# Kernel tuning notes

Hardware: AMD Instinct MI355X
Metric: run time of the kernel (lower is better)

The kernel has to match this reference:

```python
import jax, jax.numpy as jnp
import numpy as np

B, L, D = 8, 1024, 1024
H = 16
HD = D // H  # 64
R = 8


def setup_inputs() -> dict:
    key = jax.random.key(0)
    ks = jax.random.split(key, 12)
    s = 1.0 / np.sqrt(D)
    return {
        "x": jax.random.normal(ks[0], (B, L, D), dtype=jnp.float32),
        "Wq": jax.random.normal(ks[1], (D, D), dtype=jnp.float32) * s,
        "bq": jnp.zeros((D,), dtype=jnp.float32),
        "Wk": jax.random.normal(ks[2], (D, D), dtype=jnp.float32) * s,
        "bk": jnp.zeros((D,), dtype=jnp.float32),
        "Wv": jax.random.normal(ks[3], (D, D), dtype=jnp.float32) * s,
        "bv": jnp.zeros((D,), dtype=jnp.float32),
        "Wo": jax.random.normal(ks[4], (D, D), dtype=jnp.float32) * s,
        "bo": jnp.zeros((D,), dtype=jnp.float32),
        "Wrel": jax.random.normal(ks[5], (H, R), dtype=jnp.float32) * (1.0 / np.sqrt(H)),
        "brel": jnp.zeros((R,), dtype=jnp.float32),
    }


def reference(x, Wq, bq, Wk, bk, Wv, bv, Wo, bo, Wrel, brel):
    # Standard MHA with need_weights=True: full [B,H,L,L] attention matrix.
    def heads(t):  # [B,L,D] -> [B,H,L,HD]
        return t.reshape(B, L, H, HD).transpose(0, 2, 1, 3)

    q = heads(x @ Wq + bq)
    k = heads(x @ Wk + bk)
    v = heads(x @ Wv + bv)

    scores = jnp.einsum('bhld,bhmd->bhlm', q, k) / jnp.sqrt(jnp.float32(HD))
    attn = jax.nn.softmax(scores, axis=-1)  # [B,H,L,L]

    ctx = jnp.einsum('bhlm,bhmd->bhld', attn, v)
    ctx = ctx.transpose(0, 2, 1, 3).reshape(B, L, D)
    output = ctx @ Wo + bo  # [B,L,D]

    # head_patterns: mean of attention weights over (L, L) -> [B, H]
    head_patterns = attn.mean(axis=(2, 3))
    relation_scores = head_patterns @ Wrel + brel  # [B,R]
    return output, relation_scores
```

## Files before the change

### kernel.cpp

```cpp
#include <hip/hip_runtime.h>
#include <math.h>

using f32x4  = __attribute__((ext_vector_type(4))) float;
using bf16x8 = __attribute__((ext_vector_type(8))) short;
using us8    = __attribute__((ext_vector_type(8))) unsigned short;
using us4    = __attribute__((ext_vector_type(4))) unsigned short;

static __device__ __forceinline__ unsigned short f32_bf16(float f) {
    unsigned int u = __float_as_uint(f);
    u += 0x7fffu + ((u >> 16) & 1u);
    return (unsigned short)(u >> 16);
}

static __device__ __forceinline__ float fast_exp2(float x) {
    return __builtin_amdgcn_exp2f(x);
}

static __device__ __forceinline__ unsigned int bf16pk(float lo, float hi) {
    unsigned int r;
    asm("v_cvt_pk_bf16_f32 %0, %1, %2" : "=v"(r) : "v"(lo), "v"(hi));
    return r;
}

#define GLOADLDS16(src, dst)                                                          \
    __builtin_amdgcn_global_load_lds(                                                 \
        (const __attribute__((address_space(1))) void*)(src),                         \
        (__attribute__((address_space(3))) void*)(dst), 16, 0, 0)

__global__ __launch_bounds__(256) void conv_x_kernel(const float* __restrict__ x,
                                                     unsigned short* __restrict__ xb) {
    const int i = blockIdx.x * 256 + threadIdx.x;
    const float4 v = ((const float4*)x)[i];
    us4 o;
    o.x = f32_bf16(v.x); o.y = f32_bf16(v.y); o.z = f32_bf16(v.z); o.w = f32_bf16(v.w);
    ((us4*)xb)[i] = o;
}

__global__ __launch_bounds__(256) void conv_wT_kernel(
    const float* __restrict__ Wq, const float* __restrict__ Wk,
    const float* __restrict__ Wv, const float* __restrict__ Wo,
    unsigned short* __restrict__ wqkvT, unsigned short* __restrict__ woT) {
    __shared__ float t[32][33];
    const int z = blockIdx.z;
    const float* W = (z == 0) ? Wq : (z == 1) ? Wk : (z == 2) ? Wv : Wo;
    unsigned short* dst = (z < 3) ? (wqkvT + (size_t)z * 1024 * 1024) : woT;
    const int bx = blockIdx.x * 32, by = blockIdx.y * 32;
    const int tx = threadIdx.x & 31, ty = threadIdx.x >> 5;
#pragma unroll
    for (int i = ty; i < 32; i += 8)
        t[i][tx] = W[(size_t)(by + i) * 1024 + bx + tx];
    __syncthreads();
#pragma unroll
    for (int i = ty; i < 32; i += 8)
        dst[(size_t)(bx + i) * 1024 + by + tx] = f32_bf16(t[tx][i]);
}

template<int MODE>
__global__ __launch_bounds__(256) void gemm_bt_kernel(
    const unsigned short* __restrict__ A, const unsigned short* __restrict__ Bt,
    const float* __restrict__ bias_q, const float* __restrict__ bias_k,
    const float* __restrict__ bias_v,
    unsigned short* __restrict__ qkv, float* __restrict__ cout) {
    constexpr int K = 1024;
    __shared__ unsigned short As[128 * 64];
    __shared__ unsigned short Bs[128 * 64];
    const int tid = threadIdx.x;
    const int wid = tid >> 6, lane = tid & 63;
    const int bm = blockIdx.x * 128, bn = blockIdx.y * 128;
    const int wr = wid >> 1, wc = wid & 1;
    const int l15 = lane & 15, lg = lane >> 4;
    const int srow = lane >> 3;
    const int schunk = (lane & 7) ^ srow;

    f32x4 acc[4][4] = {};

    for (int kt = 0; kt < K / 64; ++kt) {
#pragma unroll
        for (int i = 0; i < 4; ++i) {
            const int li = wid * 4 + i;
            const unsigned short* sa =
                A + (size_t)(bm + li * 8 + srow) * K + kt * 64 + schunk * 8;
            GLOADLDS16(sa, &As[li * 512]);
            const unsigned short* sb =
                Bt + (size_t)(bn + li * 8 + srow) * K + kt * 64 + schunk * 8;
            GLOADLDS16(sb, &Bs[li * 512]);
        }
        __syncthreads();
#pragma unroll
        for (int ks = 0; ks < 2; ++ks) {
            bf16x8 af[4], bfr[4];
#pragma unroll
            for (int m = 0; m < 4; ++m) {
                const int row = wr * 64 + m * 16 + l15;
                const int c = (ks * 4 + lg) ^ (row & 7);
                af[m] = *(const bf16x8*)&As[row * 64 + c * 8];
            }
#pragma unroll
            for (int n = 0; n < 4; ++n) {
                const int row = wc * 64 + n * 16 + l15;
                const int c = (ks * 4 + lg) ^ (row & 7);
                bfr[n] = *(const bf16x8*)&Bs[row * 64 + c * 8];
            }
#pragma unroll
            for (int m = 0; m < 4; ++m)
#pragma unroll
                for (int n = 0; n < 4; ++n)
                    acc[m][n] = __builtin_amdgcn_mfma_f32_16x16x32_bf16(
                        bfr[n], af[m], acc[m][n], 0, 0, 0);
        }
        __syncthreads();
    }
    if constexpr (MODE == 0) {
        const int which = bn >> 10;
        const int hnb = (bn & 1023) + wc * 64;
        const float* bias = (which == 0) ? bias_q : (which == 1) ? bias_k : bias_v;
        if (which == 2) {
#pragma unroll
            for (int m = 0; m < 4; ++m) {
                const int gm = bm + wr * 64 + m * 16 + l15;
                const int b_ = gm >> 10, li2 = gm & 1023;
#pragma unroll
                for (int n = 0; n < 4; ++n) {
                    const int hn0 = hnb + n * 16 + lg * 4;
                    const float4 bb = *(const float4*)&bias[hn0];
                    const float vv[4] = {acc[m][n][0] + bb.x, acc[m][n][1] + bb.y,
                                         acc[m][n][2] + bb.z, acc[m][n][3] + bb.w};
#pragma unroll
                    for (int r = 0; r < 4; ++r) {
                        const int hn = hn0 + r;
                        qkv[16777216 +
                            ((size_t)(b_ * 16 + (hn >> 6)) * 64 + (hn & 63)) * 1024 +
                            li2] = f32_bf16(vv[r]);
                    }
                }
            }
        } else {
            const float qs = (which == 0) ? 0.125f * 1.44269504088896f : 1.0f;
#pragma unroll
            for (int m = 0; m < 4; ++m) {
                const int gm = bm + wr * 64 + m * 16 + l15;
                const size_t rowbase =
                    (((size_t)which * 128 + (gm >> 10) * 16) * 1024 + (gm & 1023)) * 64;
#pragma unroll
                for (int n = 0; n < 4; ++n) {
                    const int hn0 = hnb + n * 16 + lg * 4;
                    const float4 bb = *(const float4*)&bias[hn0];
                    const unsigned int w01 = bf16pk((acc[m][n][0] + bb.x) * qs,
                                                    (acc[m][n][1] + bb.y) * qs);
                    const unsigned int w23 = bf16pk((acc[m][n][2] + bb.z) * qs,
                                                    (acc[m][n][3] + bb.w) * qs);
                    uint2 t; t.x = w01; t.y = w23;
                    *(uint2*)&qkv[rowbase + (size_t)(hn0 >> 6) * 65536 + (hn0 & 63)] = t;
                }
            }
        }
    } else {
#pragma unroll
        for (int m = 0; m < 4; ++m) {
            const int gm = bm + wr * 64 + m * 16 + l15;
#pragma unroll
            for (int n = 0; n < 4; ++n) {
                const int gn0 = bn + wc * 64 + n * 16 + lg * 4;
                const float4 bb = *(const float4*)&bias_q[gn0];
                float4 o;
                o.x = acc[m][n][0] + bb.x; o.y = acc[m][n][1] + bb.y;
                o.z = acc[m][n][2] + bb.z; o.w = acc[m][n][3] + bb.w;
                *(float4*)&cout[(size_t)gm * 1024 + gn0] = o;
            }
        }
    }
}

__global__ __launch_bounds__(512) void attn_kernel(
    const unsigned short* __restrict__ qkv, unsigned short* __restrict__ ctx) {
    __shared__ unsigned short Ks[2][4096];
    __shared__ unsigned short VTs[2][4096];
    __shared__ unsigned short Ps[8][1024];
    const int bh = blockIdx.x, qt = blockIdx.y;
    const int b = bh >> 4, h = bh & 15;
    const unsigned short* Qp  = qkv + (size_t)bh * 65536;
    const unsigned short* Kp  = qkv + 8388608  + (size_t)bh * 65536;
    const unsigned short* VTp = qkv + 16777216 + (size_t)bh * 65536;
    const int tid = threadIdx.x, wid = tid >> 6, lane = tid & 63;
    const int l15 = lane & 15, lg = lane >> 4;
    const int q0 = qt * 128 + wid * 16;
    const int srow = lane >> 3;
    const int schunk = (lane & 7) ^ srow;

    bf16x8 qf[2];
#pragma unroll
    for (int ks = 0; ks < 2; ++ks)
        qf[ks] = *(const bf16x8*)(Qp + (size_t)(q0 + l15) * 64 + ks * 32 + lg * 8);

    f32x4 oacc[4] = {};
    float lrow = 0.f;

    int koff[4][2], poff_r[2], poff_w[4];
#pragma unroll
    for (int nf = 0; nf < 4; ++nf)
#pragma unroll
        for (int ks = 0; ks < 2; ++ks) {
            const int row = nf * 16 + l15;
            koff[nf][ks] = row * 64 + (((ks * 4 + lg) ^ (row & 7)) * 8);
        }
#pragma unroll
    for (int ks = 0; ks < 2; ++ks)
        poff_r[ks] = l15 * 64 + (((ks * 4 + lg) ^ (l15 & 7)) * 8);
#pragma unroll
    for (int nf = 0; nf < 4; ++nf) {
        const int cchunk = nf * 2 + (lg >> 1);
        poff_w[nf] = l15 * 64 + ((cchunk ^ (l15 & 7)) * 8) + (lg & 1) * 4;
    }
    unsigned short* Pw = &Ps[wid][0];

#define ATTN_STAGE(KT, BB)                                                            \
    do {                                                                              \
        GLOADLDS16(Kp + (size_t)((KT) * 64 + wid * 8 + srow) * 64 + schunk * 8,       \
                   &Ks[BB][wid * 512]);                                               \
        GLOADLDS16(VTp + (size_t)(wid * 8 + srow) * 1024 + (KT) * 64 + schunk * 8,    \
                   &VTs[BB][wid * 512]);                                              \
    } while (0)

    ATTN_STAGE(0, 0);
    for (int kt = 0; kt < 16; ++kt) {
        const int cur = kt & 1;
        if (kt < 15) {
            ATTN_STAGE(kt + 1, cur ^ 1);
            asm volatile("s_waitcnt vmcnt(2)" ::: "memory");
        } else {
            asm volatile("s_waitcnt vmcnt(0)" ::: "memory");
        }
        __builtin_amdgcn_s_barrier();

        const unsigned short* Kb = &Ks[cur][0];
        const unsigned short* Vb = &VTs[cur][0];

        f32x4 sacc[4] = {};
        __builtin_amdgcn_s_setprio(1);
#pragma unroll
        for (int ks = 0; ks < 2; ++ks)
#pragma unroll
            for (int nf = 0; nf < 4; ++nf) {
                const bf16x8 kf = *(const bf16x8*)&Kb[koff[nf][ks]];
                sacc[nf] = __builtin_amdgcn_mfma_f32_16x16x32_bf16(
                    kf, qf[ks], sacc[nf], 0, 0, 0);
            }
        __builtin_amdgcn_s_setprio(0);

        float rsa = 0.f, rsb = 0.f;
#pragma unroll
        for (int nf = 0; nf < 4; ++nf) {
            const float p0 = fast_exp2(sacc[nf][0]);
            const float p1 = fast_exp2(sacc[nf][1]);
            const float p2 = fast_exp2(sacc[nf][2]);
            const float p3 = fast_exp2(sacc[nf][3]);
            rsa += p0 + p1; rsb += p2 + p3;
            uint2 t; t.x = bf16pk(p0, p1); t.y = bf16pk(p2, p3);
            *(uint2*)&Pw[poff_w[nf]] = t;
        }
        lrow += rsa + rsb;

        __builtin_amdgcn_s_setprio(1);
#pragma unroll
        for (int ks = 0; ks < 2; ++ks) {
            const bf16x8 pf = *(const bf16x8*)&Pw[poff_r[ks]];
#pragma unroll
            for (int nf = 0; nf < 4; ++nf) {
                const bf16x8 vf = *(const bf16x8*)&Vb[koff[nf][ks]];
                oacc[nf] = __builtin_amdgcn_mfma_f32_16x16x32_bf16(
                    vf, pf, oacc[nf], 0, 0, 0);
            }
        }
        __builtin_amdgcn_s_setprio(0);

        __builtin_amdgcn_s_barrier();
    }
#undef ATTN_STAGE

    lrow += __shfl_xor(lrow, 16);
    lrow += __shfl_xor(lrow, 32);
    const float rl = 1.0f / lrow;

#pragma unroll
    for (int nf = 0; nf < 4; ++nf) {
        uint2 t;
        t.x = bf16pk(oacc[nf][0] * rl, oacc[nf][1] * rl);
        t.y = bf16pk(oacc[nf][2] * rl, oacc[nf][3] * rl);
        *(uint2*)&ctx[((size_t)(b * 1024 + q0 + l15)) * 1024 + h * 64 + nf * 16 +
                      lg * 4] = t;
    }
}

__global__ __launch_bounds__(64) void relation_kernel(
    const float* __restrict__ Wrel, const float* __restrict__ brel,
    float* __restrict__ out) {
    const int t = threadIdx.x;
    const int r = t & 7;
    float s = 0.f;
#pragma unroll
    for (int hh = 0; hh < 16; ++hh) s += Wrel[hh * 8 + r];
    out[8 * 1024 * 1024 + t] = s * (1.0f / 1024.0f) + brel[r];
}

extern "C" void kernel_launch(void* const* d_in, const int* in_sizes, int n_in,
                              void* d_out, int out_size, void* d_ws, size_t ws_size,
                              hipStream_t stream) {
    (void)in_sizes; (void)n_in; (void)out_size; (void)ws_size;
    const float* x    = (const float*)d_in[0];
    const float* Wq   = (const float*)d_in[1];
    const float* bq   = (const float*)d_in[2];
    const float* Wk   = (const float*)d_in[3];
    const float* bk   = (const float*)d_in[4];
    const float* Wv   = (const float*)d_in[5];
    const float* bv   = (const float*)d_in[6];
    const float* Wo   = (const float*)d_in[7];
    const float* bo   = (const float*)d_in[8];
    const float* Wrel = (const float*)d_in[9];
    const float* brel = (const float*)d_in[10];
    float* out = (float*)d_out;

    char* ws = (char*)d_ws;
    unsigned short* xb    = (unsigned short*)ws;
    unsigned short* wqkvT = (unsigned short*)(ws + 16777216);
    unsigned short* woT   = (unsigned short*)(ws + 16777216 + 6291456);
    unsigned short* qkv   = (unsigned short*)(ws + 16777216 + 6291456 + 2097152);
    unsigned short* ctx   = xb;

    conv_x_kernel<<<8192, 256, 0, stream>>>(x, xb);
    conv_wT_kernel<<<dim3(32, 32, 4), 256, 0, stream>>>(Wq, Wk, Wv, Wo, wqkvT, woT);
    gemm_bt_kernel<0><<<dim3(64, 24), 256, 0, stream>>>(
        xb, wqkvT, bq, bk, bv, qkv, nullptr);
    attn_kernel<<<dim3(128, 8), 512, 0, stream>>>(qkv, ctx);
    gemm_bt_kernel<1><<<dim3(64, 8), 256, 0, stream>>>(
        ctx, woT, bo, nullptr, nullptr, nullptr, out);
    relation_kernel<<<1, 64, 0, stream>>>(Wrel, brel, out);
}
```

Before: 164.0 us.

## Load V fragments straight from global into registers, drop V LDS staging

The attention kernel no longer stages the transposed V tile through double-buffered LDS. Each wave now loads its V MFMA operands directly from global memory into registers every iteration, which halves LDS use and removes the V ds_reads. The launch bounds also request 4 blocks of 512 threads per CU. In exchange, every wave of the block fetches the same V tile, so cache traffic for V rises eightfold. The __syncthreads at the loop end likely waits on the prefetched K load, reducing overlap, and the tighter register budget could force spills.

```diff
diff --git a/kernel.cpp b/kernel.cpp
--- a/kernel.cpp
+++ b/kernel.cpp
@@ -149,8 +149,8 @@
                                                     (acc[m][n][1] + bb.y) * qs);
                     const unsigned int w23 = bf16pk((acc[m][n][2] + bb.z) * qs,
                                                     (acc[m][n][3] + bb.w) * qs);
-                    uint2 t; t.x = w01; t.y = w23;
-                    *(uint2*)&qkv[rowbase + (size_t)(hn0 >> 6) * 65536 + (hn0 & 63)] = t;
+                    uint2 t2; t2.x = w01; t2.y = w23;
+                    *(uint2*)&qkv[rowbase + (size_t)(hn0 >> 6) * 65536 + (hn0 & 63)] = t2;
                 }
             }
         }
@@ -171,10 +171,9 @@
     }
 }
 
-__global__ __launch_bounds__(512) void attn_kernel(
+__global__ __launch_bounds__(512, 4) void attn_kernel(
     const unsigned short* __restrict__ qkv, unsigned short* __restrict__ ctx) {
     __shared__ unsigned short Ks[2][4096];
-    __shared__ unsigned short VTs[2][4096];
     __shared__ unsigned short Ps[8][1024];
     const int bh = blockIdx.x, qt = blockIdx.y;
     const int b = bh >> 4, h = bh & 15;
@@ -212,29 +211,27 @@
         poff_w[nf] = l15 * 64 + ((cchunk ^ (l15 & 7)) * 8) + (lg & 1) * 4;
     }
     unsigned short* Pw = &Ps[wid][0];
+    const unsigned short* vsrc = VTp + (size_t)l15 * 1024 + lg * 8;
 
 #define ATTN_STAGE(KT, BB)                                                            \
-    do {                                                                              \
-        GLOADLDS16(Kp + (size_t)((KT) * 64 + wid * 8 + srow) * 64 + schunk * 8,       \
-                   &Ks[BB][wid * 512]);                                               \
-        GLOADLDS16(VTp + (size_t)(wid * 8 + srow) * 1024 + (KT) * 64 + schunk * 8,    \
-                   &VTs[BB][wid * 512]);                                              \
-    } while (0)
+    GLOADLDS16(Kp + (size_t)((KT) * 64 + wid * 8 + srow) * 64 + schunk * 8,           \
+               &Ks[BB][wid * 512])
 
     ATTN_STAGE(0, 0);
+    __syncthreads();
     for (int kt = 0; kt < 16; ++kt) {
         const int cur = kt & 1;
-        if (kt < 15) {
-            ATTN_STAGE(kt + 1, cur ^ 1);
-            asm volatile("s_waitcnt vmcnt(2)" ::: "memory");
-        } else {
-            asm volatile("s_waitcnt vmcnt(0)" ::: "memory");
-        }
-        __builtin_amdgcn_s_barrier();
+        if (kt < 15) ATTN_STAGE(kt + 1, cur ^ 1);
+
+        bf16x8 vf[4][2];
+#pragma unroll
+        for (int nf = 0; nf < 4; ++nf)
+#pragma unroll
+            for (int ks = 0; ks < 2; ++ks)
+                vf[nf][ks] = *(const bf16x8*)(vsrc + (size_t)nf * 16384 + kt * 64 +
+                                              ks * 32);
 
         const unsigned short* Kb = &Ks[cur][0];
-        const unsigned short* Vb = &VTs[cur][0];
-
         f32x4 sacc[4] = {};
         __builtin_amdgcn_s_setprio(1);
 #pragma unroll
@@ -265,15 +262,13 @@
         for (int ks = 0; ks < 2; ++ks) {
             const bf16x8 pf = *(const bf16x8*)&Pw[poff_r[ks]];
 #pragma unroll
-            for (int nf = 0; nf < 4; ++nf) {
-                const bf16x8 vf = *(const bf16x8*)&Vb[koff[nf][ks]];
+            for (int nf = 0; nf < 4; ++nf)
                 oacc[nf] = __builtin_amdgcn_mfma_f32_16x16x32_bf16(
-                    vf, pf, oacc[nf], 0, 0, 0);
-            }
+                    vf[nf][ks], pf, oacc[nf], 0, 0, 0);
         }
         __builtin_amdgcn_s_setprio(0);
 
-        __builtin_amdgcn_s_barrier();
+        __syncthreads();
     }
 #undef ATTN_STAGE
 
```

Result: slower. 233.8 us (+42.6%).
